# Kernel optimization log

Measured on AMD Instinct MI355X. Metric: run time of the kernel, lower is better.

Reference implementation:

```python
import jax, jax.numpy as jnp
import numpy as np

N_AP, N_UE, D = 256, 1024, 64  # dimension = 64 in source

def setup_inputs() -> dict:
    key = jax.random.key(0)
    ks = jax.random.split(key, 9)
    s = 1.0 / np.sqrt(2 * D)
    return {
        "ap_hid": jax.random.normal(ks[0], (N_AP, D), jnp.float32),
        "ue_hid": jax.random.normal(ks[1], (N_UE, D), jnp.float32),
        "edge_hid": jax.random.normal(ks[2], (N_AP, N_UE, D), jnp.float32),
        "W1": jax.random.normal(ks[3], (2 * D, D), jnp.float32) * s,
        "b1": jnp.zeros((D,), jnp.float32),
        "W2": jax.random.normal(ks[4], (2 * D, D), jnp.float32) * s,
        "b2": jnp.zeros((D,), jnp.float32),
        "W3": jax.random.normal(ks[5], (2 * D, D), jnp.float32) * s,
        "b3": jnp.zeros((D,), jnp.float32),
    }

def reference(ap_hid, ue_hid, edge_hid, W1, b1, W2, b2, W3, b3):
    # edge_hid[a, u] is the feature of edge (AP a, UE u); eid is (a, u) itself.
    A, U, d = edge_hid.shape

    # reduce_func_ap: per-AP mailbox over all UE neighbors -> mlp1(cat(ap_hid, edge_hid))
    ap_in = jnp.concatenate(
        [jnp.broadcast_to(ap_hid[:, None, :], (A, U, d)), edge_hid], axis=-1)  # [A,U,2d]
    ap_res = jax.nn.relu(jnp.einsum('auk,kd->aud', ap_in, W1) + b1)            # [A,U,d]

    # reduce_func_ue: per-UE mailbox over all AP neighbors -> mlp2(cat(ue_hid, edge_hid))
    edge_ua = jnp.swapaxes(edge_hid, 0, 1)                                     # [U,A,d]
    ue_in = jnp.concatenate(
        [jnp.broadcast_to(ue_hid[:, None, :], (U, A, d)), edge_ua], axis=-1)   # [U,A,2d]
    ue_res = jax.nn.relu(jnp.einsum('uak,kd->uad', ue_in, W2) + b2)            # [U,A,d]

    # message_func_edge: for edge (a,u), sum src AP's ap_result excluding the
    # mailbox slot whose eid matches this edge, plus same for dst UE's ue_result.
    ap_sum = ap_res.sum(axis=1)   # [A,d]
    ue_sum = ue_res.sum(axis=1)   # [U,d]
    agg = (ap_sum[:, None, :] - ap_res) \
        + (ue_sum[None, :, :] - jnp.swapaxes(ue_res, 0, 1))                     # [A,U,d]

    new = jnp.einsum('auk,kd->aud', jnp.concatenate([edge_hid, agg], axis=-1), W3) + b3
    return new  # new edge 'hid' for both AP2UE and UE2AP, shape [A,U,d]
```

## Files before the change

### kernel.cpp

```cpp
#include <hip/hip_runtime.h>


#define A_N 256
#define U_N 1024

typedef short short8 __attribute__((ext_vector_type(8)));
typedef float f32x4 __attribute__((ext_vector_type(4)));

__device__ __forceinline__ unsigned short f2bf(float f) {
  unsigned int u = __float_as_uint(f);
  return (unsigned short)((u + 0x7FFFu + ((u >> 16) & 1u)) >> 16);
}

__device__ __forceinline__ f32x4 mfma16(short8 a, short8 b, f32x4 c) {
  return __builtin_amdgcn_mfma_f32_16x16x32_bf16(a, b, c, 0, 0, 0);
}

__device__ __forceinline__ void cvt16(const float4& e0, const float4& e1,
                                      const float4& e2, const float4& e3,
                                      short8& a0, short8& a1) {
  a0[0] = (short)f2bf(e0.x); a0[1] = (short)f2bf(e0.y);
  a0[2] = (short)f2bf(e0.z); a0[3] = (short)f2bf(e0.w);
  a0[4] = (short)f2bf(e1.x); a0[5] = (short)f2bf(e1.y);
  a0[6] = (short)f2bf(e1.z); a0[7] = (short)f2bf(e1.w);
  a1[0] = (short)f2bf(e2.x); a1[1] = (short)f2bf(e2.y);
  a1[2] = (short)f2bf(e2.z); a1[3] = (short)f2bf(e2.w);
  a1[4] = (short)f2bf(e3.x); a1[5] = (short)f2bf(e3.y);
  a1[6] = (short)f2bf(e3.z); a1[7] = (short)f2bf(e3.w);
}

__device__ __forceinline__ void rowmlp_row(const float* __restrict__ in,
                                           const float* __restrict__ W,
                                           const float* __restrict__ bias,
                                           float* __restrict__ out, int r, int lane) {
  float rv = in[r * 64 + lane];
  float acc = bias ? bias[lane] : 0.f;
#pragma unroll
  for (int k = 0; k < 64; k++) acc += __shfl(rv, k, 64) * W[k * 64 + lane];
  out[r * 64 + lane] = acc;
}

__global__ __launch_bounds__(256) void k_prep(
    const float* __restrict__ ap_hid, const float* __restrict__ ue_hid,
    const float* __restrict__ W1, const float* __restrict__ b1,
    const float* __restrict__ W2, const float* __restrict__ b2,
    const float* __restrict__ W3, unsigned short* __restrict__ Wt,
    float* __restrict__ c1, float* __restrict__ c2) {
  int bx = blockIdx.x, tid = threadIdx.x;
  if (bx < 64) {
    int idx = bx * 256 + tid;
    int r = idx >> 6, k = idx & 63;
    int sec = r >> 6, d = r & 63;
    float v;
    if (sec == 0)      v = W1[(64 + k) * 64 + d];
    else if (sec == 1) v = W2[(64 + k) * 64 + d];
    else if (sec == 2) v = W3[k * 64 + d];
    else               v = W3[(64 + k) * 64 + d];
    Wt[r * 64 + k] = f2bf(v);
  } else if (bx < 128) {
    int r = (bx - 64) * 4 + (tid >> 6);
    rowmlp_row(ap_hid, W1, b1, c1, r, tid & 63);
  } else {
    int r = (bx - 128) * 4 + (tid >> 6);
    rowmlp_row(ue_hid, W2, b2, c2, r, tid & 63);
  }
}

__global__ __launch_bounds__(256) void k_pass1(
    const float* __restrict__ edge, const unsigned short* __restrict__ Wt,
    const float* __restrict__ c1, const float* __restrict__ c2,
    float* __restrict__ ap_part, float* __restrict__ ue_part) {
  __shared__ float ap_l[4 * 64];
  int tid = threadIdx.x, lane = tid & 63, w = tid >> 6;
  int fr = lane & 15, fq = lane >> 4;
  int chunk = blockIdx.x >> 4;
  int panel = blockIdx.x & 15;
  int a0 = chunk * 4;
  int u0 = panel * 64;
  int urow = u0 + w * 16 + fr;
  const float* erow = edge + urow * 64 + fq * 8;

  ap_l[tid] = 0.f;
  __syncthreads();

  short8 bw[8][2];
#pragma unroll
  for (int nt = 0; nt < 8; nt++)
#pragma unroll
    for (int ks = 0; ks < 2; ks++)
      bw[nt][ks] = *(const short8*)(Wt + (nt * 16 + fr) * 64 + ks * 32 + fq * 8);

  float c2v[4][4];
#pragma unroll
  for (int j = 0; j < 4; j++)
#pragma unroll
    for (int i = 0; i < 4; i++)
      c2v[j][i] = c2[(u0 + w * 16 + fq * 4 + i) * 64 + j * 16 + fr];

  float ureg[4][4];
#pragma unroll
  for (int j = 0; j < 4; j++)
#pragma unroll
    for (int i = 0; i < 4; i++) ureg[j][i] = 0.f;

  const float* p0 = erow + a0 * 65536;
  float4 e0 = *(const float4*)(p0);
  float4 e1 = *(const float4*)(p0 + 4);
  float4 e2 = *(const float4*)(p0 + 32);
  float4 e3 = *(const float4*)(p0 + 36);
  float c1v[4];
#pragma unroll
  for (int j = 0; j < 4; j++) c1v[j] = c1[a0 * 64 + j * 16 + fr];

  for (int c = 0; c < 4; c++) {
    int a = a0 + c;
    float4 n0, n1, n2, n3;
    float nc1[4];
    if (c < 3) {
      const float* np = erow + (a + 1) * 65536;
      n0 = *(const float4*)(np);
      n1 = *(const float4*)(np + 4);
      n2 = *(const float4*)(np + 32);
      n3 = *(const float4*)(np + 36);
#pragma unroll
      for (int j = 0; j < 4; j++) nc1[j] = c1[(a + 1) * 64 + j * 16 + fr];
    }
    short8 af0, af1;
    cvt16(e0, e1, e2, e3, af0, af1);

#pragma unroll
    for (int j = 0; j < 4; j++) {
      f32x4 acc = {0.f, 0.f, 0.f, 0.f};
      acc = mfma16(af0, bw[j][0], acc);
      acc = mfma16(af1, bw[j][1], acc);
      float cv = c1v[j];
      float rs = fmaxf(acc[0] + cv, 0.f) + fmaxf(acc[1] + cv, 0.f) +
                 fmaxf(acc[2] + cv, 0.f) + fmaxf(acc[3] + cv, 0.f);
      rs += __shfl_xor(rs, 16, 64);
      rs += __shfl_xor(rs, 32, 64);
      if (lane < 16) atomicAdd(&ap_l[c * 64 + j * 16 + lane], rs);
    }
#pragma unroll
    for (int j = 0; j < 4; j++) {
      f32x4 acc = {0.f, 0.f, 0.f, 0.f};
      acc = mfma16(af0, bw[4 + j][0], acc);
      acc = mfma16(af1, bw[4 + j][1], acc);
#pragma unroll
      for (int i = 0; i < 4; i++)
        ureg[j][i] += fmaxf(acc[i] + c2v[j][i], 0.f);
    }
    if (c < 3) {
      e0 = n0; e1 = n1; e2 = n2; e3 = n3;
#pragma unroll
      for (int j = 0; j < 4; j++) c1v[j] = nc1[j];
    }
  }
#pragma unroll
  for (int j = 0; j < 4; j++)
#pragma unroll
    for (int i = 0; i < 4; i++)
      ue_part[(chunk * 1024 + u0 + w * 16 + fq * 4 + i) * 64 + j * 16 + fr] =
          ureg[j][i];
  __syncthreads();
  ap_part[(panel * 256 + a0 + w) * 64 + lane] = ap_l[tid];
}

__global__ __launch_bounds__(256) void k_mid(
    const float* __restrict__ ap_part, const float* __restrict__ ue_part,
    const float* __restrict__ W3, const float* __restrict__ b3,
    float* __restrict__ s3, float* __restrict__ s4) {
  int bx = blockIdx.x, tid = threadIdx.x, lane = tid & 63;
  const float* W3b = W3 + 4096;
  if (bx < 64) {
    int r = bx * 4 + (tid >> 6);
    float v = 0.f;
#pragma unroll
    for (int p = 0; p < 16; p++) v += ap_part[(p * 256 + r) * 64 + lane];
    float acc = 0.f;
#pragma unroll
    for (int k = 0; k < 64; k++) acc += __shfl(v, k, 64) * W3b[k * 64 + lane];
    s3[r * 64 + lane] = acc;
  } else {
    int r = (bx - 64) * 4 + (tid >> 6);
    float v = 0.f;
#pragma unroll
    for (int p = 0; p < 64; p++) v += ue_part[(p * 1024 + r) * 64 + lane];
    float acc = b3[lane];
#pragma unroll
    for (int k = 0; k < 64; k++) acc += __shfl(v, k, 64) * W3b[k * 64 + lane];
    s4[r * 64 + lane] = acc;
  }
}

__global__ __launch_bounds__(256) void k_pass2(
    const float* __restrict__ edge, const unsigned short* __restrict__ Wt,
    const float* __restrict__ c1, const float* __restrict__ c2,
    const float* __restrict__ s3, const float* __restrict__ s4,
    float* __restrict__ out) {
  __shared__ unsigned short W_lds[256 * 72];
  __shared__ unsigned short t_lds[64 * 72];
  int tid = threadIdx.x, lane = tid & 63, w = tid >> 6;
  int fr = lane & 15, fq = lane >> 4;
  int a = blockIdx.x >> 2;
  int ubase = (blockIdx.x & 3) * 256;

#pragma unroll
  for (int it = 0; it < 8; it++) {
    int r = it * 32 + (tid >> 3), seg = tid & 7;
    *(uint4*)&W_lds[r * 72 + seg * 8] = *(const uint4*)(Wt + r * 64 + seg * 8);
  }

  float c1v[4], s3v[4];
#pragma unroll
  for (int j = 0; j < 4; j++) {
    c1v[j] = c1[a * 64 + j * 16 + fr];
    s3v[j] = s3[a * 64 + j * 16 + fr];
  }

  const float* er0 = edge + (a * 1024 + ubase + w * 16 + fr) * 64 + fq * 8;
  float4 e0 = *(const float4*)(er0);
  float4 e1 = *(const float4*)(er0 + 4);
  float4 e2 = *(const float4*)(er0 + 32);
  float4 e3 = *(const float4*)(er0 + 36);

  __syncthreads();

  for (int pnl = 0; pnl < 4; pnl++) {
    int upan = ubase + pnl * 64;
    float4 n0, n1, n2, n3;
    if (pnl < 3) {
      const float* nr = edge + (a * 1024 + upan + 64 + w * 16 + fr) * 64 + fq * 8;
      n0 = *(const float4*)(nr);
      n1 = *(const float4*)(nr + 4);
      n2 = *(const float4*)(nr + 32);
      n3 = *(const float4*)(nr + 36);
    }
    float c2v[4][4], s4v[4][4];
#pragma unroll
    for (int j = 0; j < 4; j++)
#pragma unroll
      for (int i = 0; i < 4; i++) {
        int u = upan + w * 16 + fq * 4 + i;
        c2v[j][i] = c2[u * 64 + j * 16 + fr];
        s4v[j][i] = s4[u * 64 + j * 16 + fr];
      }
    short8 af0, af1;
    cvt16(e0, e1, e2, e3, af0, af1);

    f32x4 accP3[4];
#pragma unroll
    for (int j = 0; j < 4; j++) {
      const unsigned short* wr = &W_lds[(j * 16 + fr) * 72 + fq * 8];
      short8 b10 = *(const short8*)(wr);
      short8 b11 = *(const short8*)(wr + 32);
      short8 b20 = *(const short8*)(wr + 64 * 72);
      short8 b21 = *(const short8*)(wr + 64 * 72 + 32);
      short8 b30 = *(const short8*)(wr + 128 * 72);
      short8 b31 = *(const short8*)(wr + 128 * 72 + 32);
      f32x4 a1 = {0.f, 0.f, 0.f, 0.f};
      a1 = mfma16(af0, b10, a1);
      a1 = mfma16(af1, b11, a1);
      f32x4 a2 = {0.f, 0.f, 0.f, 0.f};
      a2 = mfma16(af0, b20, a2);
      a2 = mfma16(af1, b21, a2);
      f32x4 p3 = {0.f, 0.f, 0.f, 0.f};
      p3 = mfma16(af0, b30, p3);
      p3 = mfma16(af1, b31, p3);
      accP3[j] = p3;
#pragma unroll
      for (int i = 0; i < 4; i++) {
        float tv = fmaxf(a1[i] + c1v[j], 0.f) + fmaxf(a2[i] + c2v[j][i], 0.f);
        t_lds[(w * 16 + fq * 4 + i) * 72 + j * 16 + fr] = f2bf(tv);
      }
    }
    short8 tf0 = *(const short8*)&t_lds[(w * 16 + fr) * 72 + fq * 8];
    short8 tf1 = *(const short8*)&t_lds[(w * 16 + fr) * 72 + 32 + fq * 8];
#pragma unroll
    for (int j = 0; j < 4; j++) {
      const unsigned short* wr = &W_lds[(192 + j * 16 + fr) * 72 + fq * 8];
      short8 b0 = *(const short8*)(wr);
      short8 b1 = *(const short8*)(wr + 32);
      f32x4 acc = {0.f, 0.f, 0.f, 0.f};
      acc = mfma16(tf0, b0, acc);
      acc = mfma16(tf1, b1, acc);
#pragma unroll
      for (int i = 0; i < 4; i++) {
        int u = upan + w * 16 + fq * 4 + i;
        out[(a * 1024 + u) * 64 + j * 16 + fr] =
            accP3[j][i] - acc[i] + s3v[j] + s4v[j][i];
      }
    }
    if (pnl < 3) { e0 = n0; e1 = n1; e2 = n2; e3 = n3; }
  }
}

extern "C" void kernel_launch(void* const* d_in, const int* in_sizes, int n_in,
                              void* d_out, int out_size, void* d_ws, size_t ws_size,
                              hipStream_t stream) {
  const float* ap_hid = (const float*)d_in[0];
  const float* ue_hid = (const float*)d_in[1];
  const float* edge   = (const float*)d_in[2];
  const float* W1     = (const float*)d_in[3];
  const float* b1     = (const float*)d_in[4];
  const float* W2     = (const float*)d_in[5];
  const float* b2     = (const float*)d_in[6];
  const float* W3     = (const float*)d_in[7];
  const float* b3     = (const float*)d_in[8];
  float* out = (float*)d_out;

  char* ws = (char*)d_ws;
  unsigned short* Wt = (unsigned short*)ws;
  float* c1      = (float*)(ws + 32768);
  float* c2      = (float*)(ws + 98304);
  float* s3      = (float*)(ws + 360448);
  float* s4      = (float*)(ws + 425984);
  float* ap_part = (float*)(ws + 688128);
  float* ue_part = (float*)(ws + 4882432);

  k_prep<<<384, 256, 0, stream>>>(ap_hid, ue_hid, W1, b1, W2, b2, W3, Wt, c1, c2);
  k_pass1<<<1024, 256, 0, stream>>>(edge, Wt, c1, c2, ap_part, ue_part);
  k_mid<<<320, 256, 0, stream>>>(ap_part, ue_part, W3, b3, s3, s4);
  k_pass2<<<1024, 256, 0, stream>>>(edge, Wt, c1, c2, s3, s4, out);
}
```

Baseline: 171.2 us.

## Split edge passes into smaller blocks and drop LDS weight staging

The first pass now gives each block 2 APs instead of 4 and launches twice as many blocks. The mid kernel spreads each UE row's reduction over 128 partials across 4 warps, then combines them through shared memory. The second pass handles one 64-UE panel per block across 4096 blocks and reads the bf16 weights straight from global memory instead of staging them in LDS. The aim is more parallelism and occupancy with less per-block setup, at the cost of twice as much ue_part partial traffic and repeated global weight loads in every block.

```diff
diff --git a/kernel.cpp b/kernel.cpp
--- a/kernel.cpp
+++ b/kernel.cpp
@@ -70,17 +70,17 @@
     const float* __restrict__ edge, const unsigned short* __restrict__ Wt,
     const float* __restrict__ c1, const float* __restrict__ c2,
     float* __restrict__ ap_part, float* __restrict__ ue_part) {
-  __shared__ float ap_l[4 * 64];
+  __shared__ float ap_l[2 * 64];
   int tid = threadIdx.x, lane = tid & 63, w = tid >> 6;
   int fr = lane & 15, fq = lane >> 4;
   int chunk = blockIdx.x >> 4;
   int panel = blockIdx.x & 15;
-  int a0 = chunk * 4;
+  int a0 = chunk * 2;
   int u0 = panel * 64;
   int urow = u0 + w * 16 + fr;
   const float* erow = edge + urow * 64 + fq * 8;
 
-  ap_l[tid] = 0.f;
+  if (tid < 128) ap_l[tid] = 0.f;
   __syncthreads();
 
   short8 bw[8][2];
@@ -112,11 +112,11 @@
 #pragma unroll
   for (int j = 0; j < 4; j++) c1v[j] = c1[a0 * 64 + j * 16 + fr];
 
-  for (int c = 0; c < 4; c++) {
+  for (int c = 0; c < 2; c++) {
     int a = a0 + c;
     float4 n0, n1, n2, n3;
     float nc1[4];
-    if (c < 3) {
+    if (c < 1) {
       const float* np = erow + (a + 1) * 65536;
       n0 = *(const float4*)(np);
       n1 = *(const float4*)(np + 4);
@@ -149,7 +149,7 @@
       for (int i = 0; i < 4; i++)
         ureg[j][i] += fmaxf(acc[i] + c2v[j][i], 0.f);
     }
-    if (c < 3) {
+    if (c < 1) {
       e0 = n0; e1 = n1; e2 = n2; e3 = n3;
 #pragma unroll
       for (int j = 0; j < 4; j++) c1v[j] = nc1[j];
@@ -162,17 +162,18 @@
       ue_part[(chunk * 1024 + u0 + w * 16 + fq * 4 + i) * 64 + j * 16 + fr] =
           ureg[j][i];
   __syncthreads();
-  ap_part[(panel * 256 + a0 + w) * 64 + lane] = ap_l[tid];
+  if (w < 2) ap_part[(panel * 256 + a0 + w) * 64 + lane] = ap_l[w * 64 + lane];
 }
 
 __global__ __launch_bounds__(256) void k_mid(
     const float* __restrict__ ap_part, const float* __restrict__ ue_part,
     const float* __restrict__ W3, const float* __restrict__ b3,
     float* __restrict__ s3, float* __restrict__ s4) {
-  int bx = blockIdx.x, tid = threadIdx.x, lane = tid & 63;
+  __shared__ float red[4][64];
+  int bx = blockIdx.x, tid = threadIdx.x, lane = tid & 63, w = tid >> 6;
   const float* W3b = W3 + 4096;
   if (bx < 64) {
-    int r = bx * 4 + (tid >> 6);
+    int r = bx * 4 + w;
     float v = 0.f;
 #pragma unroll
     for (int p = 0; p < 16; p++) v += ap_part[(p * 256 + r) * 64 + lane];
@@ -181,14 +182,20 @@
     for (int k = 0; k < 64; k++) acc += __shfl(v, k, 64) * W3b[k * 64 + lane];
     s3[r * 64 + lane] = acc;
   } else {
-    int r = (bx - 64) * 4 + (tid >> 6);
+    int r = bx - 64;
     float v = 0.f;
 #pragma unroll
-    for (int p = 0; p < 64; p++) v += ue_part[(p * 1024 + r) * 64 + lane];
-    float acc = b3[lane];
-#pragma unroll
-    for (int k = 0; k < 64; k++) acc += __shfl(v, k, 64) * W3b[k * 64 + lane];
-    s4[r * 64 + lane] = acc;
+    for (int q = 0; q < 32; q++)
+      v += ue_part[((w * 32 + q) * 1024 + r) * 64 + lane];
+    red[w][lane] = v;
+    __syncthreads();
+    if (w == 0) {
+      float vv = red[0][lane] + red[1][lane] + red[2][lane] + red[3][lane];
+      float acc = b3[lane];
+#pragma unroll
+      for (int k = 0; k < 64; k++) acc += __shfl(vv, k, 64) * W3b[k * 64 + lane];
+      s4[r * 64 + lane] = acc;
+    }
   }
 }
 
@@ -197,18 +204,17 @@
     const float* __restrict__ c1, const float* __restrict__ c2,
     const float* __restrict__ s3, const float* __restrict__ s4,
     float* __restrict__ out) {
-  __shared__ unsigned short W_lds[256 * 72];
   __shared__ unsigned short t_lds[64 * 72];
   int tid = threadIdx.x, lane = tid & 63, w = tid >> 6;
   int fr = lane & 15, fq = lane >> 4;
-  int a = blockIdx.x >> 2;
-  int ubase = (blockIdx.x & 3) * 256;
-
-#pragma unroll
-  for (int it = 0; it < 8; it++) {
-    int r = it * 32 + (tid >> 3), seg = tid & 7;
-    *(uint4*)&W_lds[r * 72 + seg * 8] = *(const uint4*)(Wt + r * 64 + seg * 8);
-  }
+  int a = blockIdx.x >> 4;
+  int u0 = (blockIdx.x & 15) * 64;
+
+  const float* er = edge + (a * 1024 + u0 + w * 16 + fr) * 64 + fq * 8;
+  float4 e0 = *(const float4*)(er);
+  float4 e1 = *(const float4*)(er + 4);
+  float4 e2 = *(const float4*)(er + 32);
+  float4 e3 = *(const float4*)(er + 36);
 
   float c1v[4], s3v[4];
 #pragma unroll
@@ -216,81 +222,61 @@
     c1v[j] = c1[a * 64 + j * 16 + fr];
     s3v[j] = s3[a * 64 + j * 16 + fr];
   }
-
-  const float* er0 = edge + (a * 1024 + ubase + w * 16 + fr) * 64 + fq * 8;
-  float4 e0 = *(const float4*)(er0);
-  float4 e1 = *(const float4*)(er0 + 4);
-  float4 e2 = *(const float4*)(er0 + 32);
-  float4 e3 = *(const float4*)(er0 + 36);
-
-  __syncthreads();
-
-  for (int pnl = 0; pnl < 4; pnl++) {
-    int upan = ubase + pnl * 64;
-    float4 n0, n1, n2, n3;
-    if (pnl < 3) {
-      const float* nr = edge + (a * 1024 + upan + 64 + w * 16 + fr) * 64 + fq * 8;
-      n0 = *(const float4*)(nr);
-      n1 = *(const float4*)(nr + 4);
-      n2 = *(const float4*)(nr + 32);
-      n3 = *(const float4*)(nr + 36);
-    }
-    float c2v[4][4], s4v[4][4];
-#pragma unroll
-    for (int j = 0; j < 4; j++)
-#pragma unroll
-      for (int i = 0; i < 4; i++) {
-        int u = upan + w * 16 + fq * 4 + i;
-        c2v[j][i] = c2[u * 64 + j * 16 + fr];
-        s4v[j][i] = s4[u * 64 + j * 16 + fr];
-      }
-    short8 af0, af1;
-    cvt16(e0, e1, e2, e3, af0, af1);
-
-    f32x4 accP3[4];
-#pragma unroll
-    for (int j = 0; j < 4; j++) {
-      const unsigned short* wr = &W_lds[(j * 16 + fr) * 72 + fq * 8];
-      short8 b10 = *(const short8*)(wr);
-      short8 b11 = *(const short8*)(wr + 32);
-      short8 b20 = *(const short8*)(wr + 64 * 72);
-      short8 b21 = *(const short8*)(wr + 64 * 72 + 32);
-      short8 b30 = *(const short8*)(wr + 128 * 72);
-      short8 b31 = *(const short8*)(wr + 128 * 72 + 32);
-      f32x4 a1 = {0.f, 0.f, 0.f, 0.f};
-      a1 = mfma16(af0, b10, a1);
-      a1 = mfma16(af1, b11, a1);
-      f32x4 a2 = {0.f, 0.f, 0.f, 0.f};
-      a2 = mfma16(af0, b20, a2);
-      a2 = mfma16(af1, b21, a2);
-      f32x4 p3 = {0.f, 0.f, 0.f, 0.f};
-      p3 = mfma16(af0, b30, p3);
-      p3 = mfma16(af1, b31, p3);
-      accP3[j] = p3;
-#pragma unroll
-      for (int i = 0; i < 4; i++) {
-        float tv = fmaxf(a1[i] + c1v[j], 0.f) + fmaxf(a2[i] + c2v[j][i], 0.f);
-        t_lds[(w * 16 + fq * 4 + i) * 72 + j * 16 + fr] = f2bf(tv);
-      }
-    }
-    short8 tf0 = *(const short8*)&t_lds[(w * 16 + fr) * 72 + fq * 8];
-    short8 tf1 = *(const short8*)&t_lds[(w * 16 + fr) * 72 + 32 + fq * 8];
-#pragma unroll
-    for (int j = 0; j < 4; j++) {
-      const unsigned short* wr = &W_lds[(192 + j * 16 + fr) * 72 + fq * 8];
-      short8 b0 = *(const short8*)(wr);
-      short8 b1 = *(const short8*)(wr + 32);
-      f32x4 acc = {0.f, 0.f, 0.f, 0.f};
-      acc = mfma16(tf0, b0, acc);
-      acc = mfma16(tf1, b1, acc);
-#pragma unroll
-      for (int i = 0; i < 4; i++) {
-        int u = upan + w * 16 + fq * 4 + i;
-        out[(a * 1024 + u) * 64 + j * 16 + fr] =
-            accP3[j][i] - acc[i] + s3v[j] + s4v[j][i];
-      }
-    }
-    if (pnl < 3) { e0 = n0; e1 = n1; e2 = n2; e3 = n3; }
+  float c2v[4][4], s4v[4][4];
+#pragma unroll
+  for (int j = 0; j < 4; j++)
+#pragma unroll
+    for (int i = 0; i < 4; i++) {
+      int u = u0 + w * 16 + fq * 4 + i;
+      c2v[j][i] = c2[u * 64 + j * 16 + fr];
+      s4v[j][i] = s4[u * 64 + j * 16 + fr];
+    }
+
+  short8 af0, af1;
+  cvt16(e0, e1, e2, e3, af0, af1);
+
+  f32x4 accP3[4];
+#pragma unroll
+  for (int j = 0; j < 4; j++) {
+    const unsigned short* wr = Wt + (j * 16 + fr) * 64 + fq * 8;
+    short8 b10 = *(const short8*)(wr);
+    short8 b11 = *(const short8*)(wr + 32);
+    short8 b20 = *(const short8*)(wr + 64 * 64);
+    short8 b21 = *(const short8*)(wr + 64 * 64 + 32);
+    short8 b30 = *(const short8*)(wr + 128 * 64);
+    short8 b31 = *(const short8*)(wr + 128 * 64 + 32);
+    f32x4 a1 = {0.f, 0.f, 0.f, 0.f};
+    a1 = mfma16(af0, b10, a1);
+    a1 = mfma16(af1, b11, a1);
+    f32x4 a2 = {0.f, 0.f, 0.f, 0.f};
+    a2 = mfma16(af0, b20, a2);
+    a2 = mfma16(af1, b21, a2);
+    f32x4 p3 = {0.f, 0.f, 0.f, 0.f};
+    p3 = mfma16(af0, b30, p3);
+    p3 = mfma16(af1, b31, p3);
+    accP3[j] = p3;
+#pragma unroll
+    for (int i = 0; i < 4; i++) {
+      float tv = fmaxf(a1[i] + c1v[j], 0.f) + fmaxf(a2[i] + c2v[j][i], 0.f);
+      t_lds[(w * 16 + fq * 4 + i) * 72 + j * 16 + fr] = f2bf(tv);
+    }
+  }
+  short8 tf0 = *(const short8*)&t_lds[(w * 16 + fr) * 72 + fq * 8];
+  short8 tf1 = *(const short8*)&t_lds[(w * 16 + fr) * 72 + 32 + fq * 8];
+#pragma unroll
+  for (int j = 0; j < 4; j++) {
+    const unsigned short* wr = Wt + (192 + j * 16 + fr) * 64 + fq * 8;
+    short8 b0 = *(const short8*)(wr);
+    short8 b1 = *(const short8*)(wr + 32);
+    f32x4 acc = {0.f, 0.f, 0.f, 0.f};
+    acc = mfma16(tf0, b0, acc);
+    acc = mfma16(tf1, b1, acc);
+#pragma unroll
+    for (int i = 0; i < 4; i++) {
+      int u = u0 + w * 16 + fq * 4 + i;
+      out[(a * 1024 + u) * 64 + j * 16 + fr] =
+          accP3[j][i] - acc[i] + s3v[j] + s4v[j][i];
+    }
   }
 }
 
@@ -318,7 +304,7 @@
   float* ue_part = (float*)(ws + 4882432);
 
   k_prep<<<384, 256, 0, stream>>>(ap_hid, ue_hid, W1, b1, W2, b2, W3, Wt, c1, c2);
-  k_pass1<<<1024, 256, 0, stream>>>(edge, Wt, c1, c2, ap_part, ue_part);
-  k_mid<<<320, 256, 0, stream>>>(ap_part, ue_part, W3, b3, s3, s4);
-  k_pass2<<<1024, 256, 0, stream>>>(edge, Wt, c1, c2, s3, s4, out);
-}
+  k_pass1<<<2048, 256, 0, stream>>>(edge, Wt, c1, c2, ap_part, ue_part);
+  k_mid<<<1088, 256, 0, stream>>>(ap_part, ue_part, W3, b3, s3, s4);
+  k_pass2<<<4096, 256, 0, stream>>>(edge, Wt, c1, c2, s3, s4, out);
+}
```

After: 222.2 us. 29.8% more time.

## Stash bf16 edge and relu sum in pass1 so pass2 skips recomputation

Applied to the files above, without the earlier changes.

Pass1 now writes a bf16 copy of the edge tensor and the bf16 per-edge sum of the two ReLU MLP outputs to workspace. Pass2 reads these instead of re-reading fp32 edges and recomputing both MLPs, leaving only the final W3 matmul, with the weights held in registers and W3's bottom half pre-negated so the subtraction folds into one accumulator. This swaps a 64 MB fp32 edge re-read plus two MLP recomputations for 32 MB of extra bf16 writes in pass1 and 32 MB of bf16 reads in pass2, keeping total traffic about the same while cutting pass2 compute. The t value is rounded to bf16 at the same point as before.

```diff
diff --git a/kernel.cpp b/kernel.cpp
--- a/kernel.cpp
+++ b/kernel.cpp
@@ -55,7 +55,7 @@
     if (sec == 0)      v = W1[(64 + k) * 64 + d];
     else if (sec == 1) v = W2[(64 + k) * 64 + d];
     else if (sec == 2) v = W3[k * 64 + d];
-    else               v = W3[(64 + k) * 64 + d];
+    else               v = -W3[(64 + k) * 64 + d];
     Wt[r * 64 + k] = f2bf(v);
   } else if (bx < 128) {
     int r = (bx - 64) * 4 + (tid >> 6);
@@ -69,8 +69,10 @@
 __global__ __launch_bounds__(256) void k_pass1(
     const float* __restrict__ edge, const unsigned short* __restrict__ Wt,
     const float* __restrict__ c1, const float* __restrict__ c2,
-    float* __restrict__ ap_part, float* __restrict__ ue_part) {
+    float* __restrict__ ap_part, float* __restrict__ ue_part,
+    unsigned short* __restrict__ ebf, unsigned short* __restrict__ tbuf) {
   __shared__ float ap_l[4 * 64];
+  __shared__ unsigned short t_lds[64 * 72];
   int tid = threadIdx.x, lane = tid & 63, w = tid >> 6;
   int fr = lane & 15, fq = lane >> 4;
   int chunk = blockIdx.x >> 4;
@@ -128,14 +130,24 @@
     short8 af0, af1;
     cvt16(e0, e1, e2, e3, af0, af1);
 
+    {
+      unsigned short* ed = ebf + (a * 1024 + urow) * 64;
+      *(short8*)(ed + fq * 8) = af0;
+      *(short8*)(ed + 32 + fq * 8) = af1;
+    }
+
+    float tv1[4][4];
 #pragma unroll
     for (int j = 0; j < 4; j++) {
       f32x4 acc = {0.f, 0.f, 0.f, 0.f};
       acc = mfma16(af0, bw[j][0], acc);
       acc = mfma16(af1, bw[j][1], acc);
       float cv = c1v[j];
-      float rs = fmaxf(acc[0] + cv, 0.f) + fmaxf(acc[1] + cv, 0.f) +
-                 fmaxf(acc[2] + cv, 0.f) + fmaxf(acc[3] + cv, 0.f);
+      tv1[j][0] = fmaxf(acc[0] + cv, 0.f);
+      tv1[j][1] = fmaxf(acc[1] + cv, 0.f);
+      tv1[j][2] = fmaxf(acc[2] + cv, 0.f);
+      tv1[j][3] = fmaxf(acc[3] + cv, 0.f);
+      float rs = tv1[j][0] + tv1[j][1] + tv1[j][2] + tv1[j][3];
       rs += __shfl_xor(rs, 16, 64);
       rs += __shfl_xor(rs, 32, 64);
       if (lane < 16) atomicAdd(&ap_l[c * 64 + j * 16 + lane], rs);
@@ -146,8 +158,19 @@
       acc = mfma16(af0, bw[4 + j][0], acc);
       acc = mfma16(af1, bw[4 + j][1], acc);
 #pragma unroll
-      for (int i = 0; i < 4; i++)
-        ureg[j][i] += fmaxf(acc[i] + c2v[j][i], 0.f);
+      for (int i = 0; i < 4; i++) {
+        float r2 = fmaxf(acc[i] + c2v[j][i], 0.f);
+        ureg[j][i] += r2;
+        t_lds[(w * 16 + fq * 4 + i) * 72 + j * 16 + fr] = f2bf(tv1[j][i] + r2);
+      }
+    }
+    {
+      int trow = w * 16 + fr;
+      short8 tA = *(const short8*)&t_lds[trow * 72 + fq * 16];
+      short8 tB = *(const short8*)&t_lds[trow * 72 + fq * 16 + 8];
+      unsigned short* td = tbuf + (a * 1024 + u0 + trow) * 64;
+      *(short8*)(td + fq * 16) = tA;
+      *(short8*)(td + fq * 16 + 8) = tB;
     }
     if (c < 3) {
       e0 = n0; e1 = n1; e2 = n2; e3 = n3;
@@ -193,104 +216,80 @@
 }
 
 __global__ __launch_bounds__(256) void k_pass2(
-    const float* __restrict__ edge, const unsigned short* __restrict__ Wt,
-    const float* __restrict__ c1, const float* __restrict__ c2,
+    const unsigned short* __restrict__ ebf, const unsigned short* __restrict__ tbuf,
+    const unsigned short* __restrict__ Wt,
     const float* __restrict__ s3, const float* __restrict__ s4,
     float* __restrict__ out) {
-  __shared__ unsigned short W_lds[256 * 72];
-  __shared__ unsigned short t_lds[64 * 72];
   int tid = threadIdx.x, lane = tid & 63, w = tid >> 6;
   int fr = lane & 15, fq = lane >> 4;
   int a = blockIdx.x >> 2;
   int ubase = (blockIdx.x & 3) * 256;
 
-#pragma unroll
-  for (int it = 0; it < 8; it++) {
-    int r = it * 32 + (tid >> 3), seg = tid & 7;
-    *(uint4*)&W_lds[r * 72 + seg * 8] = *(const uint4*)(Wt + r * 64 + seg * 8);
-  }
-
-  float c1v[4], s3v[4];
-#pragma unroll
-  for (int j = 0; j < 4; j++) {
-    c1v[j] = c1[a * 64 + j * 16 + fr];
-    s3v[j] = s3[a * 64 + j * 16 + fr];
-  }
-
-  const float* er0 = edge + (a * 1024 + ubase + w * 16 + fr) * 64 + fq * 8;
-  float4 e0 = *(const float4*)(er0);
-  float4 e1 = *(const float4*)(er0 + 4);
-  float4 e2 = *(const float4*)(er0 + 32);
-  float4 e3 = *(const float4*)(er0 + 36);
-
-  __syncthreads();
+  short8 w3t[4][2], w3b[4][2];
+#pragma unroll
+  for (int j = 0; j < 4; j++)
+#pragma unroll
+    for (int ks = 0; ks < 2; ks++) {
+      w3t[j][ks] = *(const short8*)(Wt + (128 + j * 16 + fr) * 64 + ks * 32 + fq * 8);
+      w3b[j][ks] = *(const short8*)(Wt + (192 + j * 16 + fr) * 64 + ks * 32 + fq * 8);
+    }
+
+  float s3v[4];
+#pragma unroll
+  for (int j = 0; j < 4; j++) s3v[j] = s3[a * 64 + j * 16 + fr];
+
+  int rbase = a * 1024 + ubase + w * 16 + fr;
+
+  const unsigned short* ep = ebf + rbase * 64 + fq * 8;
+  const unsigned short* tp = tbuf + rbase * 64 + fq * 8;
+  short8 af0 = *(const short8*)(ep);
+  short8 af1 = *(const short8*)(ep + 32);
+  short8 tf0 = *(const short8*)(tp);
+  short8 tf1 = *(const short8*)(tp + 32);
+  float s4v[4][4];
+#pragma unroll
+  for (int j = 0; j < 4; j++)
+#pragma unroll
+    for (int i = 0; i < 4; i++)
+      s4v[j][i] = s4[(ubase + w * 16 + fq * 4 + i) * 64 + j * 16 + fr];
 
   for (int pnl = 0; pnl < 4; pnl++) {
     int upan = ubase + pnl * 64;
-    float4 n0, n1, n2, n3;
+    short8 na0, na1, nt0, nt1;
+    float s4n[4][4];
     if (pnl < 3) {
-      const float* nr = edge + (a * 1024 + upan + 64 + w * 16 + fr) * 64 + fq * 8;
-      n0 = *(const float4*)(nr);
-      n1 = *(const float4*)(nr + 4);
-      n2 = *(const float4*)(nr + 32);
-      n3 = *(const float4*)(nr + 36);
-    }
-    float c2v[4][4], s4v[4][4];
-#pragma unroll
-    for (int j = 0; j < 4; j++)
+      const unsigned short* nep = ebf + (rbase + (pnl + 1) * 64) * 64 + fq * 8;
+      const unsigned short* ntp = tbuf + (rbase + (pnl + 1) * 64) * 64 + fq * 8;
+      na0 = *(const short8*)(nep);
+      na1 = *(const short8*)(nep + 32);
+      nt0 = *(const short8*)(ntp);
+      nt1 = *(const short8*)(ntp + 32);
+#pragma unroll
+      for (int j = 0; j < 4; j++)
+#pragma unroll
+        for (int i = 0; i < 4; i++)
+          s4n[j][i] = s4[(upan + 64 + w * 16 + fq * 4 + i) * 64 + j * 16 + fr];
+    }
+#pragma unroll
+    for (int j = 0; j < 4; j++) {
+      f32x4 p = {0.f, 0.f, 0.f, 0.f};
+      p = mfma16(af0, w3t[j][0], p);
+      p = mfma16(af1, w3t[j][1], p);
+      p = mfma16(tf0, w3b[j][0], p);
+      p = mfma16(tf1, w3b[j][1], p);
 #pragma unroll
       for (int i = 0; i < 4; i++) {
         int u = upan + w * 16 + fq * 4 + i;
-        c2v[j][i] = c2[u * 64 + j * 16 + fr];
-        s4v[j][i] = s4[u * 64 + j * 16 + fr];
+        out[(a * 1024 + u) * 64 + j * 16 + fr] = p[i] + s3v[j] + s4v[j][i];
       }
-    short8 af0, af1;
-    cvt16(e0, e1, e2, e3, af0, af1);
-
-    f32x4 accP3[4];
-#pragma unroll
-    for (int j = 0; j < 4; j++) {
-      const unsigned short* wr = &W_lds[(j * 16 + fr) * 72 + fq * 8];
-      short8 b10 = *(const short8*)(wr);
-      short8 b11 = *(const short8*)(wr + 32);
-      short8 b20 = *(const short8*)(wr + 64 * 72);
-      short8 b21 = *(const short8*)(wr + 64 * 72 + 32);
-      short8 b30 = *(const short8*)(wr + 128 * 72);
-      short8 b31 = *(const short8*)(wr + 128 * 72 + 32);
-      f32x4 a1 = {0.f, 0.f, 0.f, 0.f};
-      a1 = mfma16(af0, b10, a1);
-      a1 = mfma16(af1, b11, a1);
-      f32x4 a2 = {0.f, 0.f, 0.f, 0.f};
-      a2 = mfma16(af0, b20, a2);
-      a2 = mfma16(af1, b21, a2);
-      f32x4 p3 = {0.f, 0.f, 0.f, 0.f};
-      p3 = mfma16(af0, b30, p3);
-      p3 = mfma16(af1, b31, p3);
-      accP3[j] = p3;
-#pragma unroll
-      for (int i = 0; i < 4; i++) {
-        float tv = fmaxf(a1[i] + c1v[j], 0.f) + fmaxf(a2[i] + c2v[j][i], 0.f);
-        t_lds[(w * 16 + fq * 4 + i) * 72 + j * 16 + fr] = f2bf(tv);
-      }
-    }
-    short8 tf0 = *(const short8*)&t_lds[(w * 16 + fr) * 72 + fq * 8];
-    short8 tf1 = *(const short8*)&t_lds[(w * 16 + fr) * 72 + 32 + fq * 8];
-#pragma unroll
-    for (int j = 0; j < 4; j++) {
-      const unsigned short* wr = &W_lds[(192 + j * 16 + fr) * 72 + fq * 8];
-      short8 b0 = *(const short8*)(wr);
-      short8 b1 = *(const short8*)(wr + 32);
-      f32x4 acc = {0.f, 0.f, 0.f, 0.f};
-      acc = mfma16(tf0, b0, acc);
-      acc = mfma16(tf1, b1, acc);
-#pragma unroll
-      for (int i = 0; i < 4; i++) {
-        int u = upan + w * 16 + fq * 4 + i;
-        out[(a * 1024 + u) * 64 + j * 16 + fr] =
-            accP3[j][i] - acc[i] + s3v[j] + s4v[j][i];
-      }
-    }
-    if (pnl < 3) { e0 = n0; e1 = n1; e2 = n2; e3 = n3; }
+    }
+    if (pnl < 3) {
+      af0 = na0; af1 = na1; tf0 = nt0; tf1 = nt1;
+#pragma unroll
+      for (int j = 0; j < 4; j++)
+#pragma unroll
+        for (int i = 0; i < 4; i++) s4v[j][i] = s4n[j][i];
+    }
   }
 }
 
@@ -309,16 +308,18 @@
   float* out = (float*)d_out;
 
   char* ws = (char*)d_ws;
-  unsigned short* Wt = (unsigned short*)ws;
+  unsigned short* Wt   = (unsigned short*)ws;
   float* c1      = (float*)(ws + 32768);
   float* c2      = (float*)(ws + 98304);
   float* s3      = (float*)(ws + 360448);
   float* s4      = (float*)(ws + 425984);
   float* ap_part = (float*)(ws + 688128);
   float* ue_part = (float*)(ws + 4882432);
+  unsigned short* ebf  = (unsigned short*)(ws + 21659648);
+  unsigned short* tbuf = (unsigned short*)(ws + 55214080);
 
   k_prep<<<384, 256, 0, stream>>>(ap_hid, ue_hid, W1, b1, W2, b2, W3, Wt, c1, c2);
-  k_pass1<<<1024, 256, 0, stream>>>(edge, Wt, c1, c2, ap_part, ue_part);
+  k_pass1<<<1024, 256, 0, stream>>>(edge, Wt, c1, c2, ap_part, ue_part, ebf, tbuf);
   k_mid<<<320, 256, 0, stream>>>(ap_part, ue_part, W3, b3, s3, s4);
-  k_pass2<<<1024, 256, 0, stream>>>(edge, Wt, c1, c2, s3, s4, out);
-}
+  k_pass2<<<1024, 256, 0, stream>>>(ebf, tbuf, Wt, s3, s4, out);
+}
```

Result: slower. 176.7 us (+3.2%).

## Fuse output projection into first edge pass and add row sums in epilogue kernel

Applied to the files above, without the earlier changes.

Moves the per-edge MLP recompute and W3 projection from the second edge pass into the first pass, so the edge tensor is read only once. The global s3/s4 terms, which depend on reductions finished later, are added by a new lightweight elementwise kernel that rereads and rewrites the output. This removes one full edge read and the redundant MLP recompute, but adds a full read-modify-write of the output plus register pressure from the extra W3 fragments kept in registers.

```diff
diff --git a/kernel.cpp b/kernel.cpp
--- a/kernel.cpp
+++ b/kernel.cpp
@@ -66,11 +66,13 @@
   }
 }
 
-__global__ __launch_bounds__(256) void k_pass1(
+__global__ __launch_bounds__(256) void k_main(
     const float* __restrict__ edge, const unsigned short* __restrict__ Wt,
     const float* __restrict__ c1, const float* __restrict__ c2,
-    float* __restrict__ ap_part, float* __restrict__ ue_part) {
+    float* __restrict__ ap_part, float* __restrict__ ue_part,
+    float* __restrict__ out) {
   __shared__ float ap_l[4 * 64];
+  __shared__ unsigned short t_lds[64 * 72];
   int tid = threadIdx.x, lane = tid & 63, w = tid >> 6;
   int fr = lane & 15, fq = lane >> 4;
   int chunk = blockIdx.x >> 4;
@@ -83,12 +85,19 @@
   ap_l[tid] = 0.f;
   __syncthreads();
 
-  short8 bw[8][2];
+  short8 bw[8][2], w3t[4][2], w3b[4][2];
 #pragma unroll
   for (int nt = 0; nt < 8; nt++)
 #pragma unroll
     for (int ks = 0; ks < 2; ks++)
       bw[nt][ks] = *(const short8*)(Wt + (nt * 16 + fr) * 64 + ks * 32 + fq * 8);
+#pragma unroll
+  for (int j = 0; j < 4; j++)
+#pragma unroll
+    for (int ks = 0; ks < 2; ks++) {
+      w3t[j][ks] = *(const short8*)(Wt + (128 + j * 16 + fr) * 64 + ks * 32 + fq * 8);
+      w3b[j][ks] = *(const short8*)(Wt + (192 + j * 16 + fr) * 64 + ks * 32 + fq * 8);
+    }
 
   float c2v[4][4];
 #pragma unroll
@@ -128,26 +137,48 @@
     short8 af0, af1;
     cvt16(e0, e1, e2, e3, af0, af1);
 
+    f32x4 accP3[4];
 #pragma unroll
     for (int j = 0; j < 4; j++) {
-      f32x4 acc = {0.f, 0.f, 0.f, 0.f};
-      acc = mfma16(af0, bw[j][0], acc);
-      acc = mfma16(af1, bw[j][1], acc);
+      f32x4 a1 = {0.f, 0.f, 0.f, 0.f};
+      a1 = mfma16(af0, bw[j][0], a1);
+      a1 = mfma16(af1, bw[j][1], a1);
       float cv = c1v[j];
-      float rs = fmaxf(acc[0] + cv, 0.f) + fmaxf(acc[1] + cv, 0.f) +
-                 fmaxf(acc[2] + cv, 0.f) + fmaxf(acc[3] + cv, 0.f);
+      float tv1[4];
+      tv1[0] = fmaxf(a1[0] + cv, 0.f);
+      tv1[1] = fmaxf(a1[1] + cv, 0.f);
+      tv1[2] = fmaxf(a1[2] + cv, 0.f);
+      tv1[3] = fmaxf(a1[3] + cv, 0.f);
+      float rs = tv1[0] + tv1[1] + tv1[2] + tv1[3];
       rs += __shfl_xor(rs, 16, 64);
       rs += __shfl_xor(rs, 32, 64);
       if (lane < 16) atomicAdd(&ap_l[c * 64 + j * 16 + lane], rs);
-    }
+      f32x4 a2 = {0.f, 0.f, 0.f, 0.f};
+      a2 = mfma16(af0, bw[4 + j][0], a2);
+      a2 = mfma16(af1, bw[4 + j][1], a2);
+#pragma unroll
+      for (int i = 0; i < 4; i++) {
+        float r2 = fmaxf(a2[i] + c2v[j][i], 0.f);
+        ureg[j][i] += r2;
+        t_lds[(w * 16 + fq * 4 + i) * 72 + j * 16 + fr] = f2bf(tv1[i] + r2);
+      }
+      f32x4 p3 = {0.f, 0.f, 0.f, 0.f};
+      p3 = mfma16(af0, w3t[j][0], p3);
+      p3 = mfma16(af1, w3t[j][1], p3);
+      accP3[j] = p3;
+    }
+    short8 tf0 = *(const short8*)&t_lds[(w * 16 + fr) * 72 + fq * 8];
+    short8 tf1 = *(const short8*)&t_lds[(w * 16 + fr) * 72 + 32 + fq * 8];
 #pragma unroll
     for (int j = 0; j < 4; j++) {
       f32x4 acc = {0.f, 0.f, 0.f, 0.f};
-      acc = mfma16(af0, bw[4 + j][0], acc);
-      acc = mfma16(af1, bw[4 + j][1], acc);
-#pragma unroll
-      for (int i = 0; i < 4; i++)
-        ureg[j][i] += fmaxf(acc[i] + c2v[j][i], 0.f);
+      acc = mfma16(tf0, w3b[j][0], acc);
+      acc = mfma16(tf1, w3b[j][1], acc);
+#pragma unroll
+      for (int i = 0; i < 4; i++) {
+        int u = u0 + w * 16 + fq * 4 + i;
+        out[(a * 1024 + u) * 64 + j * 16 + fr] = accP3[j][i] - acc[i];
+      }
     }
     if (c < 3) {
       e0 = n0; e1 = n1; e2 = n2; e3 = n3;
@@ -192,105 +223,22 @@
   }
 }
 
-__global__ __launch_bounds__(256) void k_pass2(
-    const float* __restrict__ edge, const unsigned short* __restrict__ Wt,
-    const float* __restrict__ c1, const float* __restrict__ c2,
-    const float* __restrict__ s3, const float* __restrict__ s4,
-    float* __restrict__ out) {
-  __shared__ unsigned short W_lds[256 * 72];
-  __shared__ unsigned short t_lds[64 * 72];
-  int tid = threadIdx.x, lane = tid & 63, w = tid >> 6;
-  int fr = lane & 15, fq = lane >> 4;
-  int a = blockIdx.x >> 2;
-  int ubase = (blockIdx.x & 3) * 256;
-
+__global__ __launch_bounds__(256) void k_add(
+    float* __restrict__ out, const float* __restrict__ s3,
+    const float* __restrict__ s4) {
+  int idx = blockIdx.x * 256 + threadIdx.x;
 #pragma unroll
   for (int it = 0; it < 8; it++) {
-    int r = it * 32 + (tid >> 3), seg = tid & 7;
-    *(uint4*)&W_lds[r * 72 + seg * 8] = *(const uint4*)(Wt + r * 64 + seg * 8);
-  }
-
-  float c1v[4], s3v[4];
-#pragma unroll
-  for (int j = 0; j < 4; j++) {
-    c1v[j] = c1[a * 64 + j * 16 + fr];
-    s3v[j] = s3[a * 64 + j * 16 + fr];
-  }
-
-  const float* er0 = edge + (a * 1024 + ubase + w * 16 + fr) * 64 + fq * 8;
-  float4 e0 = *(const float4*)(er0);
-  float4 e1 = *(const float4*)(er0 + 4);
-  float4 e2 = *(const float4*)(er0 + 32);
-  float4 e3 = *(const float4*)(er0 + 36);
-
-  __syncthreads();
-
-  for (int pnl = 0; pnl < 4; pnl++) {
-    int upan = ubase + pnl * 64;
-    float4 n0, n1, n2, n3;
-    if (pnl < 3) {
-      const float* nr = edge + (a * 1024 + upan + 64 + w * 16 + fr) * 64 + fq * 8;
-      n0 = *(const float4*)(nr);
-      n1 = *(const float4*)(nr + 4);
-      n2 = *(const float4*)(nr + 32);
-      n3 = *(const float4*)(nr + 36);
-    }
-    float c2v[4][4], s4v[4][4];
-#pragma unroll
-    for (int j = 0; j < 4; j++)
-#pragma unroll
-      for (int i = 0; i < 4; i++) {
-        int u = upan + w * 16 + fq * 4 + i;
-        c2v[j][i] = c2[u * 64 + j * 16 + fr];
-        s4v[j][i] = s4[u * 64 + j * 16 + fr];
-      }
-    short8 af0, af1;
-    cvt16(e0, e1, e2, e3, af0, af1);
-
-    f32x4 accP3[4];
-#pragma unroll
-    for (int j = 0; j < 4; j++) {
-      const unsigned short* wr = &W_lds[(j * 16 + fr) * 72 + fq * 8];
-      short8 b10 = *(const short8*)(wr);
-      short8 b11 = *(const short8*)(wr + 32);
-      short8 b20 = *(const short8*)(wr + 64 * 72);
-      short8 b21 = *(const short8*)(wr + 64 * 72 + 32);
-      short8 b30 = *(const short8*)(wr + 128 * 72);
-      short8 b31 = *(const short8*)(wr + 128 * 72 + 32);
-      f32x4 a1 = {0.f, 0.f, 0.f, 0.f};
-      a1 = mfma16(af0, b10, a1);
-      a1 = mfma16(af1, b11, a1);
-      f32x4 a2 = {0.f, 0.f, 0.f, 0.f};
-      a2 = mfma16(af0, b20, a2);
-      a2 = mfma16(af1, b21, a2);
-      f32x4 p3 = {0.f, 0.f, 0.f, 0.f};
-      p3 = mfma16(af0, b30, p3);
-      p3 = mfma16(af1, b31, p3);
-      accP3[j] = p3;
-#pragma unroll
-      for (int i = 0; i < 4; i++) {
-        float tv = fmaxf(a1[i] + c1v[j], 0.f) + fmaxf(a2[i] + c2v[j][i], 0.f);
-        t_lds[(w * 16 + fq * 4 + i) * 72 + j * 16 + fr] = f2bf(tv);
-      }
-    }
-    short8 tf0 = *(const short8*)&t_lds[(w * 16 + fr) * 72 + fq * 8];
-    short8 tf1 = *(const short8*)&t_lds[(w * 16 + fr) * 72 + 32 + fq * 8];
-#pragma unroll
-    for (int j = 0; j < 4; j++) {
-      const unsigned short* wr = &W_lds[(192 + j * 16 + fr) * 72 + fq * 8];
-      short8 b0 = *(const short8*)(wr);
-      short8 b1 = *(const short8*)(wr + 32);
-      f32x4 acc = {0.f, 0.f, 0.f, 0.f};
-      acc = mfma16(tf0, b0, acc);
-      acc = mfma16(tf1, b1, acc);
-#pragma unroll
-      for (int i = 0; i < 4; i++) {
-        int u = upan + w * 16 + fq * 4 + i;
-        out[(a * 1024 + u) * 64 + j * 16 + fr] =
-            accP3[j][i] - acc[i] + s3v[j] + s4v[j][i];
-      }
-    }
-    if (pnl < 3) { e0 = n0; e1 = n1; e2 = n2; e3 = n3; }
+    int f = idx + it * 524288;
+    int a = f >> 14;
+    int u = (f >> 4) & 1023;
+    int q = f & 15;
+    float4 v = *(float4*)&out[f * 4];
+    float4 x = *(const float4*)&s3[a * 64 + q * 4];
+    float4 y = *(const float4*)&s4[u * 64 + q * 4];
+    v.x += x.x + y.x; v.y += x.y + y.y;
+    v.z += x.z + y.z; v.w += x.w + y.w;
+    *(float4*)&out[f * 4] = v;
   }
 }
 
@@ -318,7 +266,7 @@
   float* ue_part = (float*)(ws + 4882432);
 
   k_prep<<<384, 256, 0, stream>>>(ap_hid, ue_hid, W1, b1, W2, b2, W3, Wt, c1, c2);
-  k_pass1<<<1024, 256, 0, stream>>>(edge, Wt, c1, c2, ap_part, ue_part);
+  k_main<<<1024, 256, 0, stream>>>(edge, Wt, c1, c2, ap_part, ue_part, out);
   k_mid<<<320, 256, 0, stream>>>(ap_part, ue_part, W3, b3, s3, s4);
-  k_pass2<<<1024, 256, 0, stream>>>(edge, Wt, c1, c2, s3, s4, out);
-}
+  k_add<<<2048, 256, 0, stream>>>(out, s3, s4);
+}
```

After: 178.2 us. 4.1% more time.
